# Kernel tuning notes

Measured on AMD Instinct MI355X. Metric: run time of the kernel, lower is better.

## Reference

```python
import jax, jax.numpy as jnp
import numpy as np

N_BITS = 8
LEVELS = 2 ** N_BITS - 1  # 255 quantization levels (asymmetric uniform)
EPS = 1e-8


def _round_ste(x):
    # straight-through round (forward: round, backward: identity)
    return x + jax.lax.stop_gradient(jnp.round(x) - x)


def _fake_quant_uniform(x):
    # dynamic per-tensor asymmetric uniform quantization (UniformQuantizer)
    xmin = jnp.min(x)
    xmax = jnp.max(x)
    scale = jnp.maximum((xmax - xmin) / LEVELS, EPS)
    zero_point = jnp.round(-xmin / scale)
    x_int = jnp.clip(_round_ste(x / scale) + zero_point, 0, LEVELS)
    return (x_int - zero_point) * scale


def setup_inputs() -> dict:
    key = jax.random.key(0)
    kA, kB = jax.random.split(key)
    A = jax.random.normal(kA, (4, 4096, 4096), dtype=jnp.float32)  # [batch, M, K]
    B = jax.random.normal(kB, (4096, 4096), dtype=jnp.float32)     # [K, N]
    return {"A": A, "B": B}


def reference(A, B):
    # QuantMatMul.forward with use_input_quant=True, use_weight_quant=True
    Aq = _fake_quant_uniform(A)
    Bq = _fake_quant_uniform(B)
    return Aq @ Bq  # [batch, M, N]
```

## Files before the change

### kernel.cpp

```cpp
#include <hip/hip_runtime.h>


#define K_DIM 4096
#define N_COLS 4096
#define M_ROWS 16384

typedef __attribute__((ext_vector_type(4))) int int4v;
typedef __attribute__((ext_vector_type(16))) int int16v;

struct QParams { float sa, zpa, sb, zpb, sab, ra, rb; int za, zb; };

static const size_t OFF_AQ = 0;
static const size_t OFF_BT = (size_t)64 << 20;
static const size_t OFF_RS = OFF_BT + ((size_t)16 << 20);
static const size_t OFF_CS = OFF_RS + (size_t)M_ROWS * 4;
static const size_t OFF_MM = OFF_CS + (size_t)N_COLS * 4;
static const size_t OFF_PR = OFF_MM + 64;

__device__ __forceinline__ unsigned enc_f(float f) {
  unsigned u = __float_as_uint(f);
  return (u & 0x80000000u) ? ~u : (u | 0x80000000u);
}
__device__ __forceinline__ float dec_f(unsigned e) {
  unsigned u = (e & 0x80000000u) ? (e & 0x7fffffffu) : ~e;
  return __uint_as_float(u);
}

__device__ __forceinline__ int quantize1(float x, float r, float zp) {
  return (int)(fminf(fmaxf(rintf(x * r) + zp, 0.0f), 255.0f)) - 128;
}

__device__ __forceinline__ void gload16(const void* g, void* l) {
  __builtin_amdgcn_global_load_lds(
      (const __attribute__((address_space(1))) unsigned int*)g,
      (__attribute__((address_space(3))) unsigned int*)l, 16, 0, 0);
}

__global__ void init_mm_k(unsigned* mm) {
  if (threadIdx.x == 0) {
    mm[0] = 0xFFFFFFFFu; mm[1] = 0u;
    mm[2] = 0xFFFFFFFFu; mm[3] = 0u;
  }
}

__global__ __launch_bounds__(256) void minmax_k(const float4* __restrict__ A,
                                                const float4* __restrict__ B,
                                                unsigned* __restrict__ mm) {
  const bool isB = blockIdx.x >= 4096;
  const float4* __restrict__ x = isB ? B : A;
  const long n4 = isB ? (long)K_DIM * N_COLS / 4 : (long)M_ROWS * K_DIM / 4;
  const int nblk = isB ? 1024 : 4096;
  const int bid = isB ? (int)blockIdx.x - 4096 : (int)blockIdx.x;
  unsigned* m = mm + (isB ? 2 : 0);

  float lo = 3.402823466e38f, hi = -3.402823466e38f;
  long i = (long)bid * blockDim.x + threadIdx.x;
  const long stride = (long)nblk * blockDim.x;
  for (; i < n4; i += stride) {
    float4 v = x[i];
    lo = fminf(lo, fminf(fminf(v.x, v.y), fminf(v.z, v.w)));
    hi = fmaxf(hi, fmaxf(fmaxf(v.x, v.y), fmaxf(v.z, v.w)));
  }
  for (int off = 32; off; off >>= 1) {
    lo = fminf(lo, __shfl_down(lo, off));
    hi = fmaxf(hi, __shfl_down(hi, off));
  }
  __shared__ float slo[4], shi[4];
  const int t = threadIdx.x;
  if ((t & 63) == 0) { slo[t >> 6] = lo; shi[t >> 6] = hi; }
  __syncthreads();
  if (t == 0) {
    for (int w = 1; w < 4; w++) { lo = fminf(lo, slo[w]); hi = fmaxf(hi, shi[w]); }
    atomicMin(&m[0], enc_f(lo));
    atomicMax(&m[1], enc_f(hi));
  }
}

__global__ void params_k(const unsigned* __restrict__ mm, QParams* __restrict__ p) {
  if (threadIdx.x != 0) return;
  const float amin = dec_f(mm[0]), amax = dec_f(mm[1]);
  const float bmin = dec_f(mm[2]), bmax = dec_f(mm[3]);
  const float sa = fmaxf((amax - amin) / 255.0f, 1e-8f);
  const float sb = fmaxf((bmax - bmin) / 255.0f, 1e-8f);
  const float zpa = rintf(-amin / sa);
  const float zpb = rintf(-bmin / sb);
  p->sa = sa; p->zpa = zpa; p->sb = sb; p->zpb = zpb;
  p->sab = sa * sb;
  p->ra = 1.0f / sa;
  p->rb = 1.0f / sb;
  p->za = (int)zpa - 128;
  p->zb = (int)zpb - 128;
}

__global__ __launch_bounds__(256) void quantA_k(const float* __restrict__ A,
                                                signed char* __restrict__ Aq,
                                                int* __restrict__ rowsum,
                                                const QParams* __restrict__ p) {
  const float ra = p->ra, zpa = p->zpa;
  const int row = blockIdx.x, t = threadIdx.x;
  const float4* src = (const float4*)(A + (size_t)row * K_DIM);
  unsigned* dst = (unsigned*)(Aq + (size_t)row * K_DIM);
  int sum = 0;
#pragma unroll
  for (int j = 0; j < 4; j++) {
    const int d = j * 256 + t;
    float4 v = src[d];
    int q0 = quantize1(v.x, ra, zpa);
    int q1 = quantize1(v.y, ra, zpa);
    int q2 = quantize1(v.z, ra, zpa);
    int q3 = quantize1(v.w, ra, zpa);
    sum += q0 + q1 + q2 + q3;
    const int dsw = (d & ~0x1C) | ((((d >> 2) ^ row) & 7) << 2);
    dst[dsw] = ((unsigned)q0 & 255u) | (((unsigned)q1 & 255u) << 8) |
               (((unsigned)q2 & 255u) << 16) | (((unsigned)q3 & 255u) << 24);
  }
  for (int off = 32; off; off >>= 1) sum += __shfl_down(sum, off);
  __shared__ int sw[4];
  if ((t & 63) == 0) sw[t >> 6] = sum;
  __syncthreads();
  if (t == 0) rowsum[row] = sw[0] + sw[1] + sw[2] + sw[3];
}

__global__ __launch_bounds__(256) void quantB_k(const float* __restrict__ B,
                                                signed char* __restrict__ Bt,
                                                const QParams* __restrict__ p) {
  const float rb = p->rb, zpb = p->zpb;
  __shared__ unsigned char s[64][72];
  const int n0 = blockIdx.x * 64, k0 = blockIdx.y * 64;
  const int t = threadIdx.x;
  const int kr = t >> 2, tl = t & 3;
  const float* rowp = B + (size_t)(k0 + kr) * N_COLS + n0;
#pragma unroll
  for (int j = 0; j < 4; j++) {
    const int fi = tl + j * 4;
    float4 v = *(const float4*)(rowp + fi * 4);
    int q0 = quantize1(v.x, rb, zpb);
    int q1 = quantize1(v.y, rb, zpb);
    int q2 = quantize1(v.z, rb, zpb);
    int q3 = quantize1(v.w, rb, zpb);
    *(unsigned*)&s[kr][fi * 4] = ((unsigned)q0 & 255u) | (((unsigned)q1 & 255u) << 8) |
                                 (((unsigned)q2 & 255u) << 16) | (((unsigned)q3 & 255u) << 24);
  }
  __syncthreads();
  const int nr = t >> 2;
  const int kb = tl * 16;
  unsigned w[4];
#pragma unroll
  for (int jj = 0; jj < 4; jj++) {
    unsigned b0 = s[kb + jj * 4 + 0][nr];
    unsigned b1 = s[kb + jj * 4 + 1][nr];
    unsigned b2 = s[kb + jj * 4 + 2][nr];
    unsigned b3 = s[kb + jj * 4 + 3][nr];
    w[jj] = b0 | (b1 << 8) | (b2 << 16) | (b3 << 24);
  }
  int4v o = {(int)w[0], (int)w[1], (int)w[2], (int)w[3]};
  const int bo = k0 + kb;
  const int bsw = (bo & ~0x70) | ((((bo >> 4) ^ nr) & 7) << 4);
  *(int4v*)(Bt + (size_t)(n0 + nr) * K_DIM + bsw) = o;
}

__global__ __launch_bounds__(256) void colsum_k(const signed char* __restrict__ Bt,
                                                int* __restrict__ colsum) {
  const int n = blockIdx.x, t = threadIdx.x;
  const int4v v = ((const int4v*)(Bt + (size_t)n * K_DIM))[t];
  int sum = 0;
#pragma unroll
  for (int c = 0; c < 4; c++) {
    unsigned w = (unsigned)v[c];
    sum += (int)(signed char)(w & 255u) + (int)(signed char)((w >> 8) & 255u) +
           (int)(signed char)((w >> 16) & 255u) + (int)(signed char)((w >> 24) & 255u);
  }
  for (int off = 32; off; off >>= 1) sum += __shfl_down(sum, off);
  __shared__ int sw[4];
  if ((t & 63) == 0) sw[t >> 6] = sum;
  __syncthreads();
  if (t == 0) colsum[n] = sw[0] + sw[1] + sw[2] + sw[3];
}

__global__ __launch_bounds__(256, 4) void gemm_k(const signed char* __restrict__ Aq,
                                                 const signed char* __restrict__ Bt,
                                                 float* __restrict__ C,
                                                 const int* __restrict__ rowsum,
                                                 const int* __restrict__ colsum,
                                                 const QParams* __restrict__ p) {
  __shared__ signed char As[128 * 128];
  __shared__ signed char Bs[128 * 128];
  const int t = threadIdx.x;
  const int m0 = blockIdx.y * 128, n0 = blockIdx.x * 128;
  const int w = t >> 6, l = t & 63;
  const int wm = (w & 1) * 64, wn = (w >> 1) * 64;
  const int r32 = l & 31, h = l >> 5;

  int16v acc[2][2] = {};

  const int off = t * 16;
  const int srow = off >> 7, scol = off & 127;
  const signed char* gA = Aq + (size_t)(m0 + srow) * K_DIM + scol;
  const signed char* gB = Bt + (size_t)(n0 + srow) * K_DIM + scol;

  const int swz = (r32 & 7);

  for (int kt = 0; kt < 32; kt++) {
    const size_t kof = (size_t)kt * 128;
#pragma unroll
    for (int r = 0; r < 4; r++) {
      gload16(gA + (size_t)(32 * r) * K_DIM + kof, As + off + r * 4096);
      gload16(gB + (size_t)(32 * r) * K_DIM + kof, Bs + off + r * 4096);
    }
    __syncthreads();
#pragma unroll
    for (int s = 0; s < 4; s++) {
      const int ca = ((2 * s + h) ^ swz) << 4;
      int4v a0 = *(const int4v*)(As + (wm + r32) * 128 + ca);
      int4v a1 = *(const int4v*)(As + (wm + 32 + r32) * 128 + ca);
      int4v b0 = *(const int4v*)(Bs + (wn + r32) * 128 + ca);
      int4v b1 = *(const int4v*)(Bs + (wn + 32 + r32) * 128 + ca);
      acc[0][0] = __builtin_amdgcn_mfma_i32_32x32x32_i8(a0, b0, acc[0][0], 0, 0, 0);
      acc[0][1] = __builtin_amdgcn_mfma_i32_32x32x32_i8(a0, b1, acc[0][1], 0, 0, 0);
      acc[1][0] = __builtin_amdgcn_mfma_i32_32x32x32_i8(a1, b0, acc[1][0], 0, 0, 0);
      acc[1][1] = __builtin_amdgcn_mfma_i32_32x32x32_i8(a1, b1, acc[1][1], 0, 0, 0);
    }
    __syncthreads();
  }

  const float sab = p->sab;
  const int za = p->za, zb = p->zb;
  const int kzz = K_DIM * za * zb;
#pragma unroll
  for (int j = 0; j < 2; j++) {
    const int col = n0 + wn + j * 32 + r32;
    const int cs = za * colsum[col];
#pragma unroll
    for (int i = 0; i < 2; i++) {
      const int rbase = m0 + wm + i * 32 + 4 * h;
#pragma unroll
      for (int r = 0; r < 16; r++) {
        const int row = rbase + (r & 3) + 8 * (r >> 2);
        const int v = acc[i][j][r] - zb * rowsum[row] - cs + kzz;
        C[(size_t)row * N_COLS + col] = sab * (float)v;
      }
    }
  }
}

extern "C" void kernel_launch(void* const* d_in, const int* in_sizes, int n_in,
                              void* d_out, int out_size, void* d_ws, size_t ws_size,
                              hipStream_t stream) {
  const float* A = (const float*)d_in[0];
  const float* B = (const float*)d_in[1];
  float* C = (float*)d_out;
  char* ws = (char*)d_ws;
  signed char* Aq = (signed char*)(ws + OFF_AQ);
  signed char* Bt = (signed char*)(ws + OFF_BT);
  int* rowsum = (int*)(ws + OFF_RS);
  int* colsum = (int*)(ws + OFF_CS);
  unsigned* mm = (unsigned*)(ws + OFF_MM);
  QParams* prm = (QParams*)(ws + OFF_PR);

  init_mm_k<<<1, 64, 0, stream>>>(mm);
  minmax_k<<<5120, 256, 0, stream>>>((const float4*)A, (const float4*)B, mm);
  params_k<<<1, 64, 0, stream>>>(mm, prm);
  quantA_k<<<M_ROWS, 256, 0, stream>>>(A, Aq, rowsum, prm);
  quantB_k<<<dim3(64, 64), 256, 0, stream>>>(B, Bt, prm);
  colsum_k<<<N_COLS, 256, 0, stream>>>(Bt, colsum);
  gemm_k<<<dim3(32, 128), 256, 0, stream>>>(Aq, Bt, C, rowsum, colsum, prm);
}
```

Measured before the change: 867.1 us.

## Double-buffer 256x256 int8 GEMM tiles with 512 threads and XCD-aware block remap

The int8 GEMM now uses 256x256 output tiles computed by 8 waves of 512 threads, with each wave holding a 128x64 accumulator. Tiles are double-buffered in 128KB of LDS so the next K-slice's global loads are issued while MFMAs run on the current one. Barriers and s_setprio bracket the MFMA groups. Block ids are remapped so neighbouring tiles land on the same XCD for L2 reuse. The aim is to hide global-load latency and raise arithmetic intensity, at the cost of higher LDS and register use, which limits occupancy.

Measured after the change: 881.8 us. No clear change (+1.7%).

```diff
diff --git a/kernel.cpp b/kernel.cpp
--- a/kernel.cpp
+++ b/kernel.cpp
@@ -177,68 +177,106 @@
   if (t == 0) colsum[n] = sw[0] + sw[1] + sw[2] + sw[3];
 }
 
-__global__ __launch_bounds__(256, 4) void gemm_k(const signed char* __restrict__ Aq,
+__device__ __forceinline__ void tile_phases(const signed char* __restrict__ gA,
+                                            const signed char* __restrict__ gB,
+                                            const signed char* cur, signed char* nxt,
+                                            size_t kof_next, bool stage,
+                                            int aoff, int boff, int off,
+                                            int h, int swz, int16v (&acc)[4][2]) {
+  const signed char* a_base = cur + aoff;
+  const signed char* b_base = cur + 32768 + boff;
+#pragma unroll
+  for (int kk = 0; kk < 4; ++kk) {
+    const int ca = ((2 * kk + h) ^ swz) << 4;
+    int4v a0 = *(const int4v*)(a_base + ca);
+    int4v a1 = *(const int4v*)(a_base + 32 * 128 + ca);
+    int4v a2 = *(const int4v*)(a_base + 64 * 128 + ca);
+    int4v a3 = *(const int4v*)(a_base + 96 * 128 + ca);
+    int4v b0 = *(const int4v*)(b_base + ca);
+    int4v b1 = *(const int4v*)(b_base + 32 * 128 + ca);
+    if (kk == 0 && stage) {
+#pragma unroll
+      for (int r = 0; r < 4; ++r) {
+        gload16(gA + (size_t)(64 * r) * K_DIM + kof_next, nxt + off + r * 8192);
+        gload16(gB + (size_t)(64 * r) * K_DIM + kof_next, nxt + 32768 + off + r * 8192);
+      }
+    }
+    __builtin_amdgcn_s_barrier();
+    __builtin_amdgcn_s_setprio(1);
+    acc[0][0] = __builtin_amdgcn_mfma_i32_32x32x32_i8(a0, b0, acc[0][0], 0, 0, 0);
+    acc[0][1] = __builtin_amdgcn_mfma_i32_32x32x32_i8(a0, b1, acc[0][1], 0, 0, 0);
+    acc[1][0] = __builtin_amdgcn_mfma_i32_32x32x32_i8(a1, b0, acc[1][0], 0, 0, 0);
+    acc[1][1] = __builtin_amdgcn_mfma_i32_32x32x32_i8(a1, b1, acc[1][1], 0, 0, 0);
+    acc[2][0] = __builtin_amdgcn_mfma_i32_32x32x32_i8(a2, b0, acc[2][0], 0, 0, 0);
+    acc[2][1] = __builtin_amdgcn_mfma_i32_32x32x32_i8(a2, b1, acc[2][1], 0, 0, 0);
+    acc[3][0] = __builtin_amdgcn_mfma_i32_32x32x32_i8(a3, b0, acc[3][0], 0, 0, 0);
+    acc[3][1] = __builtin_amdgcn_mfma_i32_32x32x32_i8(a3, b1, acc[3][1], 0, 0, 0);
+    __builtin_amdgcn_s_setprio(0);
+    if (kk < 3) __builtin_amdgcn_s_barrier();
+  }
+  __syncthreads();
+}
+
+__global__ __launch_bounds__(512, 2) void gemm_k(const signed char* __restrict__ Aq,
                                                  const signed char* __restrict__ Bt,
                                                  float* __restrict__ C,
                                                  const int* __restrict__ rowsum,
                                                  const int* __restrict__ colsum,
                                                  const QParams* __restrict__ p) {
-  __shared__ signed char As[128 * 128];
-  __shared__ signed char Bs[128 * 128];
+  __shared__ signed char lds[131072];
   const int t = threadIdx.x;
-  const int m0 = blockIdx.y * 128, n0 = blockIdx.x * 128;
+
+  const int orig = blockIdx.x;
+  const int wgid = (orig & 7) * 128 + (orig >> 3);
+  const int m0 = (wgid >> 4) * 256;
+  const int n0 = (wgid & 15) * 256;
+
   const int w = t >> 6, l = t & 63;
-  const int wm = (w & 1) * 64, wn = (w >> 1) * 64;
+  const int wm = (w >> 2) * 128;
+  const int wn = (w & 3) * 64;
   const int r32 = l & 31, h = l >> 5;
-
-  int16v acc[2][2] = {};
+  const int swz = r32 & 7;
+  const int aoff = (wm + r32) * 128;
+  const int boff = (wn + r32) * 128;
+
+  int16v acc[4][2] = {};
 
   const int off = t * 16;
   const int srow = off >> 7, scol = off & 127;
   const signed char* gA = Aq + (size_t)(m0 + srow) * K_DIM + scol;
   const signed char* gB = Bt + (size_t)(n0 + srow) * K_DIM + scol;
 
-  const int swz = (r32 & 7);
-
-  for (int kt = 0; kt < 32; kt++) {
-    const size_t kof = (size_t)kt * 128;
-#pragma unroll
-    for (int r = 0; r < 4; r++) {
-      gload16(gA + (size_t)(32 * r) * K_DIM + kof, As + off + r * 4096);
-      gload16(gB + (size_t)(32 * r) * K_DIM + kof, Bs + off + r * 4096);
-    }
-    __syncthreads();
-#pragma unroll
-    for (int s = 0; s < 4; s++) {
-      const int ca = ((2 * s + h) ^ swz) << 4;
-      int4v a0 = *(const int4v*)(As + (wm + r32) * 128 + ca);
-      int4v a1 = *(const int4v*)(As + (wm + 32 + r32) * 128 + ca);
-      int4v b0 = *(const int4v*)(Bs + (wn + r32) * 128 + ca);
-      int4v b1 = *(const int4v*)(Bs + (wn + 32 + r32) * 128 + ca);
-      acc[0][0] = __builtin_amdgcn_mfma_i32_32x32x32_i8(a0, b0, acc[0][0], 0, 0, 0);
-      acc[0][1] = __builtin_amdgcn_mfma_i32_32x32x32_i8(a0, b1, acc[0][1], 0, 0, 0);
-      acc[1][0] = __builtin_amdgcn_mfma_i32_32x32x32_i8(a1, b0, acc[1][0], 0, 0, 0);
-      acc[1][1] = __builtin_amdgcn_mfma_i32_32x32x32_i8(a1, b1, acc[1][1], 0, 0, 0);
-    }
-    __syncthreads();
+  signed char* s0 = lds;
+  signed char* s1 = lds + 65536;
+
+#pragma unroll
+  for (int r = 0; r < 4; ++r) {
+    gload16(gA + (size_t)(64 * r) * K_DIM, s0 + off + r * 8192);
+    gload16(gB + (size_t)(64 * r) * K_DIM, s0 + 32768 + off + r * 8192);
+  }
+  __syncthreads();
+
+  for (int kth = 0; kth < 16; ++kth) {
+    const int t1 = 2 * kth + 1;
+    tile_phases(gA, gB, s0, s1, (size_t)(t1)*128, true, aoff, boff, off, h, swz, acc);
+    tile_phases(gA, gB, s1, s0, (size_t)(t1 + 1) * 128, t1 + 1 < 32, aoff, boff, off, h, swz, acc);
   }
 
   const float sab = p->sab;
   const int za = p->za, zb = p->zb;
   const int kzz = K_DIM * za * zb;
-#pragma unroll
-  for (int j = 0; j < 2; j++) {
-    const int col = n0 + wn + j * 32 + r32;
-    const int cs = za * colsum[col];
-#pragma unroll
-    for (int i = 0; i < 2; i++) {
-      const int rbase = m0 + wm + i * 32 + 4 * h;
-#pragma unroll
-      for (int r = 0; r < 16; r++) {
-        const int row = rbase + (r & 3) + 8 * (r >> 2);
-        const int v = acc[i][j][r] - zb * rowsum[row] - cs + kzz;
-        C[(size_t)row * N_COLS + col] = sab * (float)v;
-      }
+  const int col0 = n0 + wn + r32;
+  const int cs0 = za * colsum[col0];
+  const int cs1 = za * colsum[col0 + 32];
+#pragma unroll
+  for (int m = 0; m < 4; ++m) {
+    const int rbase = m0 + wm + m * 32 + 4 * h;
+#pragma unroll
+    for (int r = 0; r < 16; ++r) {
+      const int row = rbase + (r & 3) + 8 * (r >> 2);
+      const int base = kzz - zb * rowsum[row];
+      C[(size_t)row * N_COLS + col0] = sab * (float)(acc[m][0][r] + base - cs0);
+      C[(size_t)row * N_COLS + col0 + 32] = sab * (float)(acc[m][1][r] + base - cs1);
     }
   }
 }
@@ -263,5 +301,5 @@
   quantA_k<<<M_ROWS, 256, 0, stream>>>(A, Aq, rowsum, prm);
   quantB_k<<<dim3(64, 64), 256, 0, stream>>>(B, Bt, prm);
   colsum_k<<<N_COLS, 256, 0, stream>>>(Bt, colsum);
-  gemm_k<<<dim3(32, 128), 256, 0, stream>>>(Aq, Bt, C, rowsum, colsum, prm);
-}
+  gemm_k<<<1024, 512, 0, stream>>>(Aq, Bt, C, rowsum, colsum, prm);
+}
```

## Double-buffer int8 GEMM with 256x128 tiles, XCD-aware block remap, and inline qparams

Applied to the files above, without the earlier changes.

Rewrites the int8 GEMM to use 512-thread blocks on a 256x128 output tile with a 64-wide K step. LDS is double-buffered so global-to-LDS loads of the next stage overlap the MFMA work on the current one, and MFMA sections run under raised s_setprio. Blocks are remapped across XCDs to improve L2 reuse, and the swizzle moves from the quantize kernels into the load addressing. The params_k launch is dropped: each kernel recomputes the quantization parameters from the min/max words, which costs one fewer launch but adds redundant scalar math. The main aim is to hide memory latency and cut per-iteration barrier stalls, at the risk of higher register and LDS pressure limiting occupancy.

Measured after the change: 894.5 us. 3.2% more time.

```diff
diff --git a/kernel.cpp b/kernel.cpp
--- a/kernel.cpp
+++ b/kernel.cpp
@@ -7,15 +7,12 @@
 
 typedef __attribute__((ext_vector_type(4))) int int4v;
 typedef __attribute__((ext_vector_type(16))) int int16v;
-
-struct QParams { float sa, zpa, sb, zpb, sab, ra, rb; int za, zb; };
 
 static const size_t OFF_AQ = 0;
 static const size_t OFF_BT = (size_t)64 << 20;
 static const size_t OFF_RS = OFF_BT + ((size_t)16 << 20);
 static const size_t OFF_CS = OFF_RS + (size_t)M_ROWS * 4;
 static const size_t OFF_MM = OFF_CS + (size_t)N_COLS * 4;
-static const size_t OFF_PR = OFF_MM + 64;
 
 __device__ __forceinline__ unsigned enc_f(float f) {
   unsigned u = __float_as_uint(f);
@@ -34,6 +31,19 @@
   __builtin_amdgcn_global_load_lds(
       (const __attribute__((address_space(1))) unsigned int*)g,
       (__attribute__((address_space(3))) unsigned int*)l, 16, 0, 0);
+}
+
+__device__ __forceinline__ void qparams_a(const unsigned* mm, float& ra, float& zpa) {
+  const float amin = dec_f(mm[0]), amax = dec_f(mm[1]);
+  const float sa = fmaxf((amax - amin) / 255.0f, 1e-8f);
+  zpa = rintf(-amin / sa);
+  ra = 1.0f / sa;
+}
+__device__ __forceinline__ void qparams_b(const unsigned* mm, float& rb, float& zpb) {
+  const float bmin = dec_f(mm[2]), bmax = dec_f(mm[3]);
+  const float sb = fmaxf((bmax - bmin) / 255.0f, 1e-8f);
+  zpb = rintf(-bmin / sb);
+  rb = 1.0f / sb;
 }
 
 __global__ void init_mm_k(unsigned* mm) {
@@ -76,27 +86,12 @@
   }
 }
 
-__global__ void params_k(const unsigned* __restrict__ mm, QParams* __restrict__ p) {
-  if (threadIdx.x != 0) return;
-  const float amin = dec_f(mm[0]), amax = dec_f(mm[1]);
-  const float bmin = dec_f(mm[2]), bmax = dec_f(mm[3]);
-  const float sa = fmaxf((amax - amin) / 255.0f, 1e-8f);
-  const float sb = fmaxf((bmax - bmin) / 255.0f, 1e-8f);
-  const float zpa = rintf(-amin / sa);
-  const float zpb = rintf(-bmin / sb);
-  p->sa = sa; p->zpa = zpa; p->sb = sb; p->zpb = zpb;
-  p->sab = sa * sb;
-  p->ra = 1.0f / sa;
-  p->rb = 1.0f / sb;
-  p->za = (int)zpa - 128;
-  p->zb = (int)zpb - 128;
-}
-
 __global__ __launch_bounds__(256) void quantA_k(const float* __restrict__ A,
                                                 signed char* __restrict__ Aq,
                                                 int* __restrict__ rowsum,
-                                                const QParams* __restrict__ p) {
-  const float ra = p->ra, zpa = p->zpa;
+                                                const unsigned* __restrict__ mm) {
+  float ra, zpa;
+  qparams_a(mm, ra, zpa);
   const int row = blockIdx.x, t = threadIdx.x;
   const float4* src = (const float4*)(A + (size_t)row * K_DIM);
   unsigned* dst = (unsigned*)(Aq + (size_t)row * K_DIM);
@@ -110,9 +105,8 @@
     int q2 = quantize1(v.z, ra, zpa);
     int q3 = quantize1(v.w, ra, zpa);
     sum += q0 + q1 + q2 + q3;
-    const int dsw = (d & ~0x1C) | ((((d >> 2) ^ row) & 7) << 2);
-    dst[dsw] = ((unsigned)q0 & 255u) | (((unsigned)q1 & 255u) << 8) |
-               (((unsigned)q2 & 255u) << 16) | (((unsigned)q3 & 255u) << 24);
+    dst[d] = ((unsigned)q0 & 255u) | (((unsigned)q1 & 255u) << 8) |
+             (((unsigned)q2 & 255u) << 16) | (((unsigned)q3 & 255u) << 24);
   }
   for (int off = 32; off; off >>= 1) sum += __shfl_down(sum, off);
   __shared__ int sw[4];
@@ -123,8 +117,9 @@
 
 __global__ __launch_bounds__(256) void quantB_k(const float* __restrict__ B,
                                                 signed char* __restrict__ Bt,
-                                                const QParams* __restrict__ p) {
-  const float rb = p->rb, zpb = p->zpb;
+                                                const unsigned* __restrict__ mm) {
+  float rb, zpb;
+  qparams_b(mm, rb, zpb);
   __shared__ unsigned char s[64][72];
   const int n0 = blockIdx.x * 64, k0 = blockIdx.y * 64;
   const int t = threadIdx.x;
@@ -154,9 +149,7 @@
     w[jj] = b0 | (b1 << 8) | (b2 << 16) | (b3 << 24);
   }
   int4v o = {(int)w[0], (int)w[1], (int)w[2], (int)w[3]};
-  const int bo = k0 + kb;
-  const int bsw = (bo & ~0x70) | ((((bo >> 4) ^ nr) & 7) << 4);
-  *(int4v*)(Bt + (size_t)(n0 + nr) * K_DIM + bsw) = o;
+  *(int4v*)(Bt + (size_t)(n0 + nr) * K_DIM + (k0 + kb)) = o;
 }
 
 __global__ __launch_bounds__(256) void colsum_k(const signed char* __restrict__ Bt,
@@ -177,68 +170,109 @@
   if (t == 0) colsum[n] = sw[0] + sw[1] + sw[2] + sw[3];
 }
 
-__global__ __launch_bounds__(256, 4) void gemm_k(const signed char* __restrict__ Aq,
+__global__ __launch_bounds__(512, 4) void gemm_k(const signed char* __restrict__ Aq,
                                                  const signed char* __restrict__ Bt,
                                                  float* __restrict__ C,
                                                  const int* __restrict__ rowsum,
                                                  const int* __restrict__ colsum,
-                                                 const QParams* __restrict__ p) {
-  __shared__ signed char As[128 * 128];
-  __shared__ signed char Bs[128 * 128];
+                                                 const unsigned* __restrict__ mm) {
+  __shared__ signed char lds[49152];
   const int t = threadIdx.x;
-  const int m0 = blockIdx.y * 128, n0 = blockIdx.x * 128;
+
+  const int orig = blockIdx.x;
+  const int wgid = (orig & 7) * 256 + (orig >> 3);
+  const int m0 = (wgid >> 5) * 256;
+  const int n0 = (wgid & 31) * 128;
+
   const int w = t >> 6, l = t & 63;
-  const int wm = (w & 1) * 64, wn = (w >> 1) * 64;
+  const int wm = (w >> 2) * 128;
+  const int wn = (w & 3) * 32;
   const int r32 = l & 31, h = l >> 5;
-
-  int16v acc[2][2] = {};
-
-  const int off = t * 16;
-  const int srow = off >> 7, scol = off & 127;
-  const signed char* gA = Aq + (size_t)(m0 + srow) * K_DIM + scol;
-  const signed char* gB = Bt + (size_t)(n0 + srow) * K_DIM + scol;
-
-  const int swz = (r32 & 7);
-
-  for (int kt = 0; kt < 32; kt++) {
-    const size_t kof = (size_t)kt * 128;
-#pragma unroll
-    for (int r = 0; r < 4; r++) {
-      gload16(gA + (size_t)(32 * r) * K_DIM + kof, As + off + r * 4096);
-      gload16(gB + (size_t)(32 * r) * K_DIM + kof, Bs + off + r * 4096);
-    }
-    __syncthreads();
-#pragma unroll
-    for (int s = 0; s < 4; s++) {
-      const int ca = ((2 * s + h) ^ swz) << 4;
-      int4v a0 = *(const int4v*)(As + (wm + r32) * 128 + ca);
-      int4v a1 = *(const int4v*)(As + (wm + 32 + r32) * 128 + ca);
-      int4v b0 = *(const int4v*)(Bs + (wn + r32) * 128 + ca);
-      int4v b1 = *(const int4v*)(Bs + (wn + 32 + r32) * 128 + ca);
-      acc[0][0] = __builtin_amdgcn_mfma_i32_32x32x32_i8(a0, b0, acc[0][0], 0, 0, 0);
-      acc[0][1] = __builtin_amdgcn_mfma_i32_32x32x32_i8(a0, b1, acc[0][1], 0, 0, 0);
-      acc[1][0] = __builtin_amdgcn_mfma_i32_32x32x32_i8(a1, b0, acc[1][0], 0, 0, 0);
-      acc[1][1] = __builtin_amdgcn_mfma_i32_32x32x32_i8(a1, b1, acc[1][1], 0, 0, 0);
-    }
-    __syncthreads();
-  }
-
-  const float sab = p->sab;
-  const int za = p->za, zb = p->zb;
+  const int u = r32 >> 2, c4 = (r32 & 3) * 4;
+
+  unsigned aAddr[4][2], bAddr[2];
+#pragma unroll
+  for (int m = 0; m < 4; ++m)
+#pragma unroll
+    for (int kk = 0; kk < 2; ++kk)
+      aAddr[m][kk] = (unsigned)(((wm + 32 * m) >> 2) + u) * 256 +
+                     (unsigned)(((c4 + 2 * kk + h) ^ u) << 4);
+#pragma unroll
+  for (int kk = 0; kk < 2; ++kk)
+    bAddr[kk] = 16384u + (unsigned)(8 * (w & 3) + u) * 256 +
+                (unsigned)(((c4 + 2 * kk + h) ^ u) << 4);
+
+  const int bs_ = t & 15, Rq = t >> 4;
+  const int b16 = bs_ ^ (Rq & 7);
+  const int sc = b16 >> 2, slb = b16 & 3;
+  const signed char* pA0 = Aq + (size_t)(m0 + 4 * Rq + sc) * K_DIM + slb * 16;
+  const signed char* pA1 = pA0 + (size_t)128 * K_DIM;
+  const signed char* pB  = Bt + (size_t)(n0 + 4 * Rq + sc) * K_DIM + slb * 16;
+
+  int16v acc[4] = {};
+
+#define STAGE(NXT) do {                                   \
+    gload16(pA0, lds + (NXT) + t * 16);                   \
+    gload16(pA1, lds + (NXT) + 8192 + t * 16);            \
+    gload16(pB,  lds + (NXT) + 16384 + t * 16);           \
+    pA0 += 64; pA1 += 64; pB += 64; } while (0)
+
+#define MFMA4(A0, A1, A2, A3, B0)                                            \
+    __builtin_amdgcn_s_setprio(1);                                           \
+    acc[0] = __builtin_amdgcn_mfma_i32_32x32x32_i8(A0, B0, acc[0], 0, 0, 0); \
+    acc[1] = __builtin_amdgcn_mfma_i32_32x32x32_i8(A1, B0, acc[1], 0, 0, 0); \
+    acc[2] = __builtin_amdgcn_mfma_i32_32x32x32_i8(A2, B0, acc[2], 0, 0, 0); \
+    acc[3] = __builtin_amdgcn_mfma_i32_32x32x32_i8(A3, B0, acc[3], 0, 0, 0); \
+    __builtin_amdgcn_s_setprio(0);
+
+#define COMP(CUR) do {                                                \
+    int4v b0 = *(const int4v*)(lds + (CUR) + bAddr[0]);               \
+    int4v a0 = *(const int4v*)(lds + (CUR) + aAddr[0][0]);            \
+    int4v a1 = *(const int4v*)(lds + (CUR) + aAddr[1][0]);            \
+    int4v a2 = *(const int4v*)(lds + (CUR) + aAddr[2][0]);            \
+    int4v a3 = *(const int4v*)(lds + (CUR) + aAddr[3][0]);            \
+    MFMA4(a0, a1, a2, a3, b0)                                         \
+    b0 = *(const int4v*)(lds + (CUR) + bAddr[1]);                     \
+    a0 = *(const int4v*)(lds + (CUR) + aAddr[0][1]);                  \
+    a1 = *(const int4v*)(lds + (CUR) + aAddr[1][1]);                  \
+    a2 = *(const int4v*)(lds + (CUR) + aAddr[2][1]);                  \
+    a3 = *(const int4v*)(lds + (CUR) + aAddr[3][1]);                  \
+    MFMA4(a0, a1, a2, a3, b0)                                         \
+  } while (0)
+
+  STAGE(0);
+  __syncthreads();
+
+#pragma unroll 1
+  for (int it = 0; it < 31; ++it) {
+    STAGE(24576); COMP(0);     __syncthreads();
+    STAGE(0);     COMP(24576); __syncthreads();
+  }
+  STAGE(24576); COMP(0); __syncthreads();
+  COMP(24576);
+
+#undef STAGE
+#undef MFMA4
+#undef COMP
+
+  const float amin = dec_f(mm[0]), amax = dec_f(mm[1]);
+  const float bmin = dec_f(mm[2]), bmax = dec_f(mm[3]);
+  const float sa = fmaxf((amax - amin) / 255.0f, 1e-8f);
+  const float sb = fmaxf((bmax - bmin) / 255.0f, 1e-8f);
+  const int za = (int)rintf(-amin / sa) - 128;
+  const int zb = (int)rintf(-bmin / sb) - 128;
+  const float sab = sa * sb;
   const int kzz = K_DIM * za * zb;
-#pragma unroll
-  for (int j = 0; j < 2; j++) {
-    const int col = n0 + wn + j * 32 + r32;
-    const int cs = za * colsum[col];
-#pragma unroll
-    for (int i = 0; i < 2; i++) {
-      const int rbase = m0 + wm + i * 32 + 4 * h;
-#pragma unroll
-      for (int r = 0; r < 16; r++) {
-        const int row = rbase + (r & 3) + 8 * (r >> 2);
-        const int v = acc[i][j][r] - zb * rowsum[row] - cs + kzz;
-        C[(size_t)row * N_COLS + col] = sab * (float)v;
-      }
+  const int col = n0 + wn + r32;
+  const int cs = za * colsum[col];
+#pragma unroll
+  for (int m = 0; m < 4; ++m) {
+    const int rbase = m0 + wm + m * 32 + 4 * h;
+#pragma unroll
+    for (int r = 0; r < 16; ++r) {
+      const int row = rbase + (r & 3) + 8 * (r >> 2);
+      const int v = acc[m][r] - zb * rowsum[row] - cs + kzz;
+      C[(size_t)row * N_COLS + col] = sab * (float)v;
     }
   }
 }
@@ -255,13 +289,11 @@
   int* rowsum = (int*)(ws + OFF_RS);
   int* colsum = (int*)(ws + OFF_CS);
   unsigned* mm = (unsigned*)(ws + OFF_MM);
-  QParams* prm = (QParams*)(ws + OFF_PR);
 
   init_mm_k<<<1, 64, 0, stream>>>(mm);
   minmax_k<<<5120, 256, 0, stream>>>((const float4*)A, (const float4*)B, mm);
-  params_k<<<1, 64, 0, stream>>>(mm, prm);
-  quantA_k<<<M_ROWS, 256, 0, stream>>>(A, Aq, rowsum, prm);
-  quantB_k<<<dim3(64, 64), 256, 0, stream>>>(B, Bt, prm);
+  quantA_k<<<M_ROWS, 256, 0, stream>>>(A, Aq, rowsum, mm);
+  quantB_k<<<dim3(64, 64), 256, 0, stream>>>(B, Bt, mm);
   colsum_k<<<N_COLS, 256, 0, stream>>>(Bt, colsum);
-  gemm_k<<<dim3(32, 128), 256, 0, stream>>>(Aq, Bt, C, rowsum, colsum, prm);
-}
+  gemm_k<<<2048, 512, 0, stream>>>(Aq, Bt, C, rowsum, colsum, mm);
+}
```
